# Kernel optimization log

Hardware: AMD Instinct MI355X
Metric: run time of the kernel (lower is better)

Reference implementation:

```python
import jax, jax.numpy as jnp
import numpy as np

PLANE_AXES = jnp.array([[[0., 1., 0.], [1., 0., 0.], [0., 0., 1.]],
                        [[0., 0., 1.], [1., 0., 0.], [0., 1., 0.]],
                        [[0., 1., 0.], [0., 0., 1.], [1., 0., 0.]]], dtype=jnp.float32)


def setup_inputs() -> dict:
    key = jax.random.key(0)
    k1, k2 = jax.random.split(key)
    M, C, R = 1048576, 32, 512
    coords = jax.random.uniform(k1, (M, 3), jnp.float32, -1.0, 1.0)
    triplane = jax.random.normal(k2, (1, 3, C, R, R), jnp.float32) * 0.1
    return {"coords": coords, "triplane": triplane}


def _bilinear_sample(plane, x, y):
    # plane: [C, R, R]; x, y: [M] pixel coords (align_corners=True mapping applied).
    # Matches torch grid_sample(mode='bilinear', padding_mode='zeros', align_corners=True).
    R = plane.shape[-1]
    x0 = jnp.floor(x)
    y0 = jnp.floor(y)
    x0i = x0.astype(jnp.int32)
    y0i = y0.astype(jnp.int32)
    wx1 = x - x0
    wx0 = 1.0 - wx1
    wy1 = y - y0
    wy0 = 1.0 - wy1

    def tap(xi, yi, w):
        valid = ((xi >= 0) & (xi < R) & (yi >= 0) & (yi < R)).astype(plane.dtype)
        xc = jnp.clip(xi, 0, R - 1)
        yc = jnp.clip(yi, 0, R - 1)
        return plane[:, yc, xc] * (w * valid)  # [C, M]

    return (tap(x0i, y0i, wx0 * wy0) + tap(x0i + 1, y0i, wx1 * wy0)
            + tap(x0i, y0i + 1, wx0 * wy1) + tap(x0i + 1, y0i + 1, wx1 * wy1))


def reference(coords, triplane):
    # coords: [M, 3]; triplane: [1, 3, C, R, R]
    _, P, C, R, _ = triplane.shape
    planes = jnp.clip(triplane.reshape(P, C, R, R), -1.0, 1.0)
    inv = jnp.linalg.inv(PLANE_AXES)  # [3, 3, 3]
    # project_onto_planes: bmm(coords, inv_planes), keep first two coords (x, y)
    proj = jnp.einsum('mc,pcd->pmd', coords, inv)[..., :2]  # [3, M, 2]
    px = (proj[..., 0] + 1.0) * 0.5 * (R - 1)  # align_corners=True
    py = (proj[..., 1] + 1.0) * 0.5 * (R - 1)
    feat = jax.vmap(_bilinear_sample)(planes, px, py)  # [3, C, M]
    return feat.sum(0).T  # [M, C] — sum across the 3 planes
```

## Files before the change

kernel.cpp:

```cpp
#include <hip/hip_runtime.h>
#include <hip/hip_bf16.h>
#include <stdint.h>

#define RES 512
#define CH  32
#define NP  3
#define NTEX (NP * RES * RES)
#define NT2  (NTEX / 2)
#define WS_BYTES ((size_t)NTEX * CH * sizeof(uint16_t))

typedef float vfloat4 __attribute__((ext_vector_type(4)));

static __device__ __forceinline__ uint16_t f2bf(float f) {
    union { float f; uint32_t u; } v; v.f = f;
    uint32_t u = v.u;
    uint32_t r = (u + 0x7fffu + ((u >> 16) & 1u)) >> 16;
    return (uint16_t)r;
}

__global__ __launch_bounds__(256) void k_transpose(const float* __restrict__ tri,
                                                   uint16_t* __restrict__ ws) {
    int t2 = blockIdx.x * 256 + threadIdx.x;
    if (t2 >= NT2) return;
    int xp = t2 & (RES / 2 - 1);
    int y  = (t2 >> 8) & (RES - 1);
    int p  = t2 >> 17;
    int x  = xp * 2;
    const float* src = tri + (size_t)p * CH * RES * RES + (size_t)y * RES + x;
    uint32_t pa[16], pb[16];
#pragma unroll
    for (int i = 0; i < 16; ++i) {
        float2 f0 = *(const float2*)&src[(size_t)(2 * i + 0) * (RES * RES)];
        float2 f1 = *(const float2*)&src[(size_t)(2 * i + 1) * (RES * RES)];
        float a0 = fminf(1.f, fmaxf(-1.f, f0.x));
        float a1 = fminf(1.f, fmaxf(-1.f, f1.x));
        float b0 = fminf(1.f, fmaxf(-1.f, f0.y));
        float b1 = fminf(1.f, fmaxf(-1.f, f1.y));
        pa[i] = (uint32_t)f2bf(a0) | ((uint32_t)f2bf(a1) << 16);
        pb[i] = (uint32_t)f2bf(b0) | ((uint32_t)f2bf(b1) << 16);
    }
    uint4* dst = (uint4*)(ws + (size_t)(2 * t2) * CH);
#pragma unroll
    for (int i = 0; i < 4; ++i)
        dst[i] = make_uint4(pa[4 * i], pa[4 * i + 1], pa[4 * i + 2], pa[4 * i + 3]);
#pragma unroll
    for (int i = 0; i < 4; ++i)
        dst[4 + i] = make_uint4(pb[4 * i], pb[4 * i + 1], pb[4 * i + 2], pb[4 * i + 3]);
}

__global__ __launch_bounds__(256) void k_gather(const float* __restrict__ coords,
                                                const uint16_t* __restrict__ ws,
                                                float* __restrict__ out, int M) {
    int tid = threadIdx.x;
    int sub = tid & 3;
    int m = blockIdx.x * 64 + (tid >> 2);
    if (m >= M) return;
    float cx = coords[3 * m + 0];
    float cy = coords[3 * m + 1];
    float cz = coords[3 * m + 2];

    float acc[8];
#pragma unroll
    for (int c = 0; c < 8; ++c) acc[c] = 0.f;

    float us[3] = {cy, cz, cy};
    float vs[3] = {cx, cx, cz};

#pragma unroll
    for (int p = 0; p < 3; ++p) {
        float px = (us[p] + 1.f) * (0.5f * (RES - 1));
        float py = (vs[p] + 1.f) * (0.5f * (RES - 1));
        float x0f = floorf(px), y0f = floorf(py);
        int x0 = (int)x0f, y0 = (int)y0f;
        float wx1 = px - x0f, wx0 = 1.f - wx1;
        float wy1 = py - y0f, wy0 = 1.f - wy1;
        int   xs[2]  = {x0, x0 + 1};
        int   ys[2]  = {y0, y0 + 1};
        float wxv[2] = {wx0, wx1};
        float wyv[2] = {wy0, wy1};
#pragma unroll
        for (int j = 0; j < 2; ++j) {
#pragma unroll
            for (int i = 0; i < 2; ++i) {
                int xi = xs[i], yi = ys[j];
                bool valid = (xi >= 0) & (xi < RES) & (yi >= 0) & (yi < RES);
                int xc = min(max(xi, 0), RES - 1);
                int yc = min(max(yi, 0), RES - 1);
                float w = valid ? (wxv[i] * wyv[j]) : 0.f;
                const uint4* tp = (const uint4*)(ws + (((size_t)p * RES + yc) * RES + xc) * CH
                                                 + (size_t)sub * 8);
                uint4 d = *tp;
                uint32_t vv[4] = {d.x, d.y, d.z, d.w};
#pragma unroll
                for (int e = 0; e < 4; ++e) {
                    union { uint32_t u; float f; } lo, hi;
                    lo.u = vv[e] << 16;
                    hi.u = vv[e] & 0xffff0000u;
                    acc[2 * e + 0] += w * lo.f;
                    acc[2 * e + 1] += w * hi.f;
                }
            }
        }
    }

    vfloat4* dst = (vfloat4*)(out + (size_t)m * CH + (size_t)sub * 8);
    vfloat4 v0 = {acc[0], acc[1], acc[2], acc[3]};
    vfloat4 v1 = {acc[4], acc[5], acc[6], acc[7]};
    __builtin_nontemporal_store(v0, dst);
    __builtin_nontemporal_store(v1, dst + 1);
}

__global__ __launch_bounds__(256) void k_gather_direct(const float* __restrict__ coords,
                                                       const float* __restrict__ tri,
                                                       float* __restrict__ out, int M) {
    int m = blockIdx.x * 256 + threadIdx.x;
    if (m >= M) return;
    float cx = coords[3 * m + 0];
    float cy = coords[3 * m + 1];
    float cz = coords[3 * m + 2];
    float acc[CH];
#pragma unroll
    for (int c = 0; c < CH; ++c) acc[c] = 0.f;
    float us[3] = {cy, cz, cy};
    float vs[3] = {cx, cx, cz};
    for (int p = 0; p < 3; ++p) {
        float px = (us[p] + 1.f) * (0.5f * (RES - 1));
        float py = (vs[p] + 1.f) * (0.5f * (RES - 1));
        float x0f = floorf(px), y0f = floorf(py);
        int x0 = (int)x0f, y0 = (int)y0f;
        float wx1 = px - x0f, wx0 = 1.f - wx1;
        float wy1 = py - y0f, wy0 = 1.f - wy1;
        int   xs[2]  = {x0, x0 + 1};
        int   ys[2]  = {y0, y0 + 1};
        float wxv[2] = {wx0, wx1};
        float wyv[2] = {wy0, wy1};
        for (int j = 0; j < 2; ++j)
            for (int i = 0; i < 2; ++i) {
                int xi = xs[i], yi = ys[j];
                bool valid = (xi >= 0) & (xi < RES) & (yi >= 0) & (yi < RES);
                int xc = min(max(xi, 0), RES - 1);
                int yc = min(max(yi, 0), RES - 1);
                float w = valid ? (wxv[i] * wyv[j]) : 0.f;
                const float* base = tri + ((size_t)p * CH) * RES * RES + (size_t)yc * RES + xc;
#pragma unroll
                for (int c = 0; c < CH; ++c) {
                    float v = base[(size_t)c * RES * RES];
                    v = fminf(1.f, fmaxf(-1.f, v));
                    acc[c] += w * v;
                }
            }
    }
    float4* dst = (float4*)(out + (size_t)m * CH);
#pragma unroll
    for (int i = 0; i < 8; ++i)
        dst[i] = make_float4(acc[4 * i], acc[4 * i + 1], acc[4 * i + 2], acc[4 * i + 3]);
}

extern "C" void kernel_launch(void* const* d_in, const int* in_sizes, int n_in,
                              void* d_out, int out_size, void* d_ws, size_t ws_size,
                              hipStream_t stream) {
    const float* coords = (const float*)d_in[0];
    const float* tri    = (const float*)d_in[1];
    float* out          = (float*)d_out;
    int M = in_sizes[0] / 3;

    if (ws_size >= WS_BYTES) {
        uint16_t* ws = (uint16_t*)d_ws;
        k_transpose<<<(NT2 + 255) / 256, 256, 0, stream>>>(tri, ws);
        k_gather<<<(M + 63) / 64, 256, 0, stream>>>(coords, ws, out, M);
    } else {
        k_gather_direct<<<(M + 255) / 256, 256, 0, stream>>>(coords, tri, out, M);
    }
}
```

Measured before the change: 406.3 us.

## Bin query points spatially via counting sort before texture gather

Adds a 16^3 spatial binning pass (histogram, scan, scatter) that reorders query points by 3D cell before the bilinear gather, so neighbouring threads hit nearby texels in the transposed bf16 triplane and get better cache reuse. The gather then writes results back to each point's original index. This costs four extra small kernels, an extra 16 MB write and read of the sorted coordinates, and atomics, plus scattered output stores.

```diff
diff --git a/kernel.cpp b/kernel.cpp
--- a/kernel.cpp
+++ b/kernel.cpp
@@ -7,7 +7,9 @@
 #define NP  3
 #define NTEX (NP * RES * RES)
 #define NT2  (NTEX / 2)
-#define WS_BYTES ((size_t)NTEX * CH * sizeof(uint16_t))
+#define TEX_BYTES ((size_t)NTEX * CH * sizeof(uint16_t))
+#define BGRID 16
+#define NBIN  (BGRID * BGRID * BGRID)
 
 typedef float vfloat4 __attribute__((ext_vector_type(4)));
 
@@ -16,6 +18,14 @@
     uint32_t u = v.u;
     uint32_t r = (u + 0x7fffu + ((u >> 16) & 1u)) >> 16;
     return (uint16_t)r;
+}
+
+static __device__ __forceinline__ int binq(float c) {
+    int v = (int)floorf((c + 1.f) * (BGRID * 0.5f));
+    return min(BGRID - 1, max(0, v));
+}
+static __device__ __forceinline__ int bin_of(float cx, float cy, float cz) {
+    return (binq(cz) * BGRID + binq(cy)) * BGRID + binq(cx);
 }
 
 __global__ __launch_bounds__(256) void k_transpose(const float* __restrict__ tri,
@@ -48,16 +58,78 @@
         dst[4 + i] = make_uint4(pb[4 * i], pb[4 * i + 1], pb[4 * i + 2], pb[4 * i + 3]);
 }
 
-__global__ __launch_bounds__(256) void k_gather(const float* __restrict__ coords,
-                                                const uint16_t* __restrict__ ws,
-                                                float* __restrict__ out, int M) {
+__global__ __launch_bounds__(256) void k_zero(uint32_t* __restrict__ hist) {
+    int i = blockIdx.x * 256 + threadIdx.x;
+    if (i < NBIN) hist[i] = 0;
+}
+
+__global__ __launch_bounds__(256) void k_hist(const float* __restrict__ coords,
+                                              uint32_t* __restrict__ hist, int M) {
+    __shared__ uint32_t hl[NBIN];
+    for (int i = threadIdx.x; i < NBIN; i += 256) hl[i] = 0;
+    __syncthreads();
+    int base = blockIdx.x * 1024 + threadIdx.x;
+#pragma unroll
+    for (int k = 0; k < 4; ++k) {
+        int m = base + k * 256;
+        if (m < M) {
+            float cx = coords[3 * m + 0];
+            float cy = coords[3 * m + 1];
+            float cz = coords[3 * m + 2];
+            atomicAdd(&hl[bin_of(cx, cy, cz)], 1u);
+        }
+    }
+    __syncthreads();
+    for (int i = threadIdx.x; i < NBIN; i += 256) {
+        uint32_t v = hl[i];
+        if (v) atomicAdd(&hist[i], v);
+    }
+}
+
+__global__ __launch_bounds__(256) void k_scan(const uint32_t* __restrict__ hist,
+                                              uint32_t* __restrict__ cursor) {
+    __shared__ uint32_t part[256];
     int tid = threadIdx.x;
-    int sub = tid & 3;
-    int m = blockIdx.x * 64 + (tid >> 2);
+    int b0 = tid * (NBIN / 256);
+    uint32_t loc[NBIN / 256];
+    uint32_t s = 0;
+#pragma unroll
+    for (int k = 0; k < NBIN / 256; ++k) { loc[k] = hist[b0 + k]; s += loc[k]; }
+    part[tid] = s;
+    __syncthreads();
+    for (int off = 1; off < 256; off <<= 1) {
+        uint32_t v = (tid >= off) ? part[tid - off] : 0u;
+        __syncthreads();
+        part[tid] += v;
+        __syncthreads();
+    }
+    uint32_t run = part[tid] - s;
+#pragma unroll
+    for (int k = 0; k < NBIN / 256; ++k) { cursor[b0 + k] = run; run += loc[k]; }
+}
+
+__global__ __launch_bounds__(256) void k_scatter(const float* __restrict__ coords,
+                                                 uint32_t* __restrict__ cursor,
+                                                 float4* __restrict__ csort, int M) {
+    int m = blockIdx.x * 256 + threadIdx.x;
     if (m >= M) return;
     float cx = coords[3 * m + 0];
     float cy = coords[3 * m + 1];
     float cz = coords[3 * m + 2];
+    uint32_t pos = atomicAdd(&cursor[bin_of(cx, cy, cz)], 1u);
+    csort[pos] = make_float4(cx, cy, cz, __uint_as_float((uint32_t)m));
+}
+
+__global__ __launch_bounds__(256) void k_gather_sorted(const float4* __restrict__ csort,
+                                                       const uint16_t* __restrict__ tex,
+                                                       float* __restrict__ out, int M) {
+    int tid = threadIdx.x;
+    int sub = tid & 3;
+    int i = blockIdx.x * 64 + (tid >> 2);
+    if (i >= M) return;
+    float4 c4 = csort[i];
+    float cx = c4.x, cy = c4.y, cz = c4.z;
+    uint32_t mo = __float_as_uint(c4.w);
 
     float acc[8];
 #pragma unroll
@@ -81,6 +153,65 @@
 #pragma unroll
         for (int j = 0; j < 2; ++j) {
 #pragma unroll
+            for (int i2 = 0; i2 < 2; ++i2) {
+                int xi = xs[i2], yi = ys[j];
+                bool valid = (xi >= 0) & (xi < RES) & (yi >= 0) & (yi < RES);
+                int xc = min(max(xi, 0), RES - 1);
+                int yc = min(max(yi, 0), RES - 1);
+                float w = valid ? (wxv[i2] * wyv[j]) : 0.f;
+                const uint4* tp = (const uint4*)(tex + (((size_t)p * RES + yc) * RES + xc) * CH
+                                                 + (size_t)sub * 8);
+                uint4 d = *tp;
+                uint32_t vv[4] = {d.x, d.y, d.z, d.w};
+#pragma unroll
+                for (int e = 0; e < 4; ++e) {
+                    union { uint32_t u; float f; } lo, hi;
+                    lo.u = vv[e] << 16;
+                    hi.u = vv[e] & 0xffff0000u;
+                    acc[2 * e + 0] += w * lo.f;
+                    acc[2 * e + 1] += w * hi.f;
+                }
+            }
+        }
+    }
+
+    vfloat4* dst = (vfloat4*)(out + (size_t)mo * CH + (size_t)sub * 8);
+    vfloat4 v0 = {acc[0], acc[1], acc[2], acc[3]};
+    vfloat4 v1 = {acc[4], acc[5], acc[6], acc[7]};
+    __builtin_nontemporal_store(v0, dst);
+    __builtin_nontemporal_store(v1, dst + 1);
+}
+
+__global__ __launch_bounds__(256) void k_gather(const float* __restrict__ coords,
+                                                const uint16_t* __restrict__ ws,
+                                                float* __restrict__ out, int M) {
+    int tid = threadIdx.x;
+    int sub = tid & 3;
+    int m = blockIdx.x * 64 + (tid >> 2);
+    if (m >= M) return;
+    float cx = coords[3 * m + 0];
+    float cy = coords[3 * m + 1];
+    float cz = coords[3 * m + 2];
+    float acc[8];
+#pragma unroll
+    for (int c = 0; c < 8; ++c) acc[c] = 0.f;
+    float us[3] = {cy, cz, cy};
+    float vs[3] = {cx, cx, cz};
+#pragma unroll
+    for (int p = 0; p < 3; ++p) {
+        float px = (us[p] + 1.f) * (0.5f * (RES - 1));
+        float py = (vs[p] + 1.f) * (0.5f * (RES - 1));
+        float x0f = floorf(px), y0f = floorf(py);
+        int x0 = (int)x0f, y0 = (int)y0f;
+        float wx1 = px - x0f, wx0 = 1.f - wx1;
+        float wy1 = py - y0f, wy0 = 1.f - wy1;
+        int   xs[2]  = {x0, x0 + 1};
+        int   ys[2]  = {y0, y0 + 1};
+        float wxv[2] = {wx0, wx1};
+        float wyv[2] = {wy0, wy1};
+#pragma unroll
+        for (int j = 0; j < 2; ++j) {
+#pragma unroll
             for (int i = 0; i < 2; ++i) {
                 int xi = xs[i], yi = ys[j];
                 bool valid = (xi >= 0) & (xi < RES) & (yi >= 0) & (yi < RES);
@@ -102,7 +233,6 @@
             }
         }
     }
-
     vfloat4* dst = (vfloat4*)(out + (size_t)m * CH + (size_t)sub * 8);
     vfloat4 v0 = {acc[0], acc[1], acc[2], acc[3]};
     vfloat4 v1 = {acc[4], acc[5], acc[6], acc[7]};
@@ -164,7 +294,23 @@
     float* out          = (float*)d_out;
     int M = in_sizes[0] / 3;
 
-    if (ws_size >= WS_BYTES) {
+    size_t off_csort  = TEX_BYTES;
+    size_t off_hist   = off_csort + (size_t)M * 16;
+    size_t off_cursor = off_hist + (size_t)NBIN * 4;
+    size_t need_full  = off_cursor + (size_t)NBIN * 4;
+
+    if (ws_size >= need_full) {
+        uint16_t* tex    = (uint16_t*)d_ws;
+        float4*   csort  = (float4*)((char*)d_ws + off_csort);
+        uint32_t* hist   = (uint32_t*)((char*)d_ws + off_hist);
+        uint32_t* cursor = (uint32_t*)((char*)d_ws + off_cursor);
+        k_transpose<<<(NT2 + 255) / 256, 256, 0, stream>>>(tri, (uint16_t*)d_ws);
+        k_zero<<<(NBIN + 255) / 256, 256, 0, stream>>>(hist);
+        k_hist<<<(M + 1023) / 1024, 256, 0, stream>>>(coords, hist, M);
+        k_scan<<<1, 256, 0, stream>>>(hist, cursor);
+        k_scatter<<<(M + 255) / 256, 256, 0, stream>>>(coords, cursor, csort, M);
+        k_gather_sorted<<<(M + 63) / 64, 256, 0, stream>>>(csort, tex, out, M);
+    } else if (ws_size >= TEX_BYTES) {
         uint16_t* ws = (uint16_t*)d_ws;
         k_transpose<<<(NT2 + 255) / 256, 256, 0, stream>>>(tri, ws);
         k_gather<<<(M + 63) / 64, 256, 0, stream>>>(coords, ws, out, M);
```

Result: slower. 435.9 us (+7.3%).
